# Kernel optimization log

Hardware: AMD Instinct MI355X
Metric: run time of the kernel (lower is better)

## Reference

```python
import jax, jax.numpy as jnp
import numpy as np


def setup_inputs() -> dict:
    key = jax.random.key(0)
    ks = jax.random.split(key, 6)
    B, n_tok, n_RoI = 8, 64, 100
    T_hidden, I_hidden = 768, 1024
    P = I_hidden // 2  # projection = 512
    s_q = 1.0 / np.sqrt(T_hidden)
    s_k = 1.0 / np.sqrt(I_hidden)
    s_w = 1.0 / np.sqrt(P)
    return {
        "encT": jax.random.normal(ks[0], (B, n_tok, T_hidden), jnp.float32),
        "encI": jax.random.normal(ks[1], (B, n_RoI, I_hidden), jnp.float32),
        "mask": jnp.zeros((B, 1, n_tok, n_RoI), jnp.float32),
        "Wq": jax.random.normal(ks[2], (T_hidden, P), jnp.float32) * s_q,
        "bq": jnp.zeros((P,), jnp.float32),
        "Wk": jax.random.normal(ks[3], (I_hidden, P), jnp.float32) * s_k,
        "bk": jnp.zeros((P,), jnp.float32),
        "w": jax.random.normal(ks[4], (P,), jnp.float32) * s_w,
        "b": jnp.zeros((1,), jnp.float32),
    }


def reference(encT, encI, mask, Wq, bq, Wk, bk, w, b):
    # Q_mlp / K_mlp: Linear + exact GELU (torch nn.GELU default)
    q = jax.nn.gelu(jnp.einsum('bth,hp->btp', encT, Wq) + bq, approximate=False)  # [B,T,P]
    k = jax.nn.gelu(jnp.einsum('brh,hp->brp', encI, Wk) + bk, approximate=False)  # [B,R,P]
    # broadcast add (instead of repeat/view), tanh, then Linear(P,1)
    fusion = jnp.tanh(q[:, :, None, :] + k[:, None, :, :])  # [B,T,R,P]
    logits = jnp.einsum('btrp,p->btr', fusion, w) + b[0]      # [B,T,R]
    return logits + jnp.squeeze(mask, axis=1)
```

## Files before the change

kernel.cpp:

```cpp
#include <hip/hip_runtime.h>
#include <hip/hip_fp16.h>
#include <math.h>

#define B_  8
#define T_  64
#define R_  100
#define TH_ 768
#define IH_ 1024
#define P_  512
#define N_  512

#define CTANH 2.88539008177792681f

typedef short short8  __attribute__((ext_vector_type(8)));
typedef float floatx4 __attribute__((ext_vector_type(4)));

__device__ __forceinline__ ushort f2bf(float f) {
  union { float f; unsigned int u; } v; v.f = f;
  unsigned int r = v.u + 0x7FFFu + ((v.u >> 16) & 1u);
  return (ushort)(r >> 16);
}

#define PADK 40

__global__ __launch_bounds__(1024) void mfma_linear_gelu_sk4(
    const float* __restrict__ encT, const float* __restrict__ Wq,
    const float* __restrict__ bq, __half* __restrict__ qout,
    const float* __restrict__ encI, const float* __restrict__ Wk,
    const float* __restrict__ bk, __half* __restrict__ kout) {
  const int rt = blockIdx.y;
  const bool isQ = rt < 8;
  const float* __restrict__ X = isQ ? encT : encI;
  const float* __restrict__ W = isQ ? Wq : Wk;
  const float* __restrict__ bias = isQ ? bq : bk;
  __half* __restrict__ Y = isQ ? qout : kout;
  const int M    = isQ ? (B_ * T_) : (B_ * R_);
  const int KDIM = isQ ? TH_ : IH_;
  const int row0 = (isQ ? rt : (rt - 8)) * 64;
  const int col0 = blockIdx.x * 32;
  const int kq   = KDIM >> 2;
  const int ntiles = kq / 32;

  __shared__ ushort As[4][64 * PADK];
  __shared__ ushort Bs[4][32 * PADK];
  __shared__ float  red[2][64 * 33];

  const int tid = threadIdx.x;
  const int sp  = tid >> 8;
  const int t   = tid & 255;
  const int kbase = sp * kq;

  const int arow = t >> 2;
  const int akq  = (t & 3) * 8;
  const int arowc = min(row0 + arow, M - 1);
  const float* __restrict__ Xp = X + (size_t)arowc * KDIM + kbase + akq;

  const int bkp = (t >> 4) * 2;
  const int bn2 = (t & 15) * 2;
  const float* __restrict__ Wp = W + (size_t)(kbase + bkp) * N_ + col0 + bn2;

  const int wv = t >> 6;
  const int lane = t & 63;
  const int wm = wv * 16;
  const int l15 = lane & 15;
  const int q8  = (lane >> 4) * 8;
  const int q4  = (lane >> 4) * 4;

  floatx4 acc0 = {0.f,0.f,0.f,0.f}, acc1 = {0.f,0.f,0.f,0.f};

  float4 a0 = *(const float4*)(Xp);
  float4 a1 = *(const float4*)(Xp + 4);
  float2 b0 = *(const float2*)(Wp);
  float2 b1 = *(const float2*)(Wp + N_);

  for (int kt = 0; kt < ntiles; ++kt) {
    {
      short8 pk;
      pk[0] = (short)f2bf(a0.x); pk[1] = (short)f2bf(a0.y);
      pk[2] = (short)f2bf(a0.z); pk[3] = (short)f2bf(a0.w);
      pk[4] = (short)f2bf(a1.x); pk[5] = (short)f2bf(a1.y);
      pk[6] = (short)f2bf(a1.z); pk[7] = (short)f2bf(a1.w);
      *(short8*)&As[sp][arow * PADK + akq] = pk;
    }
    {
      unsigned int p0 = (unsigned int)f2bf(b0.x) | ((unsigned int)f2bf(b1.x) << 16);
      unsigned int p1 = (unsigned int)f2bf(b0.y) | ((unsigned int)f2bf(b1.y) << 16);
      *(unsigned int*)&Bs[sp][(bn2 + 0) * PADK + bkp] = p0;
      *(unsigned int*)&Bs[sp][(bn2 + 1) * PADK + bkp] = p1;
    }
    __syncthreads();

    if (kt + 1 < ntiles) {
      const int kb = (kt + 1) * 32;
      a0 = *(const float4*)(Xp + kb);
      a1 = *(const float4*)(Xp + kb + 4);
      b0 = *(const float2*)(Wp + (size_t)kb * N_);
      b1 = *(const float2*)(Wp + (size_t)(kb + 1) * N_);
    }

    short8 af  = *(const short8*)&As[sp][(wm + l15) * PADK + q8];
    short8 bf0 = *(const short8*)&Bs[sp][(l15) * PADK + q8];
    short8 bf1 = *(const short8*)&Bs[sp][(16 + l15) * PADK + q8];
    acc0 = __builtin_amdgcn_mfma_f32_16x16x32_bf16(af, bf0, acc0, 0, 0, 0);
    acc1 = __builtin_amdgcn_mfma_f32_16x16x32_bf16(af, bf1, acc1, 0, 0, 0);
    __syncthreads();
  }

  if (sp >= 2) {
    float* L = red[sp - 2];
    #pragma unroll
    for (int j = 0; j < 4; ++j) {
      L[(wm + q4 + j) * 33 + l15]      = acc0[j];
      L[(wm + q4 + j) * 33 + 16 + l15] = acc1[j];
    }
  }
  __syncthreads();
  if (sp < 2) {
    const float* L = red[sp];
    #pragma unroll
    for (int j = 0; j < 4; ++j) {
      acc0[j] += L[(wm + q4 + j) * 33 + l15];
      acc1[j] += L[(wm + q4 + j) * 33 + 16 + l15];
    }
  }
  __syncthreads();
  if (sp == 1) {
    float* L = red[0];
    #pragma unroll
    for (int j = 0; j < 4; ++j) {
      L[(wm + q4 + j) * 33 + l15]      = acc0[j];
      L[(wm + q4 + j) * 33 + 16 + l15] = acc1[j];
    }
  }
  __syncthreads();
  if (sp == 0) {
    const float* L = red[0];
    const float is2 = 0.70710678118654752f;
    const float bia0 = bias[col0 + l15];
    const float bia1 = bias[col0 + 16 + l15];
    #pragma unroll
    for (int j = 0; j < 4; ++j) {
      const int row = row0 + wm + q4 + j;
      if (row < M) {
        float v0 = acc0[j] + L[(wm + q4 + j) * 33 + l15] + bia0;
        float v1 = acc1[j] + L[(wm + q4 + j) * 33 + 16 + l15] + bia1;
        v0 = CTANH * 0.5f * v0 * (1.f + erff(v0 * is2));
        v1 = CTANH * 0.5f * v1 * (1.f + erff(v1 * is2));
        Y[(size_t)row * N_ + col0 + l15]      = __float2half(v0);
        Y[(size_t)row * N_ + col0 + 16 + l15] = __float2half(v1);
      }
    }
  }
}

__global__ __launch_bounds__(256) void fuse_kernel_h(
    const __half* __restrict__ q, const __half* __restrict__ k,
    const float* __restrict__ w, const float* __restrict__ bscalar,
    const float* __restrict__ mask, float* __restrict__ out) {
  const int bt = blockIdx.x;
  const int wave = threadIdx.x >> 6;
  const int rg = blockIdx.y * 4 + wave;
  if (rg >= 25) return;
  const int lane = threadIdx.x & 63;
  const int sub  = lane >> 4;
  const int pi   = lane & 15;
  const int r = rg * 4 + sub;
  const int b = bt >> 6;

  const __half* __restrict__ qp = q + (size_t)bt * P_ + pi * 8;
  const __half* __restrict__ kp = k + (size_t)(b * R_ + r) * P_ + pi * 8;
  const float* __restrict__ wp = w + pi * 8;

  float acc0 = 0.f, acc1 = 0.f;
  #pragma unroll
  for (int i = 0; i < 4; ++i) {
    union { float4 f; __half2 h[4]; } qu, ku;
    qu.f = *(const float4*)(qp + i * 128);
    ku.f = *(const float4*)(kp + i * 128);
    float4 w0 = *(const float4*)(wp + i * 128);
    float4 w1 = *(const float4*)(wp + i * 128 + 4);
    #pragma unroll
    for (int e = 0; e < 4; ++e) {
      __half2 s = __hadd2(qu.h[e], ku.h[e]);
      float x0 = __low2float(s);
      float x1 = __high2float(s);
      float d0 = __builtin_amdgcn_rcpf(1.f + __builtin_amdgcn_exp2f(x0));
      float d1 = __builtin_amdgcn_rcpf(1.f + __builtin_amdgcn_exp2f(x1));
      float s0 = fmaf(-2.f, d0, 1.f);
      float s1 = fmaf(-2.f, d1, 1.f);
      const float we0 = (e == 0) ? w0.x : (e == 1) ? w0.z : (e == 2) ? w1.x : w1.z;
      const float we1 = (e == 0) ? w0.y : (e == 1) ? w0.w : (e == 2) ? w1.y : w1.w;
      acc0 = fmaf(we0, s0, acc0);
      acc1 = fmaf(we1, s1, acc1);
    }
  }
  float acc = acc0 + acc1;
  #pragma unroll
  for (int off = 1; off < 16; off <<= 1) acc += __shfl_xor(acc, off, 64);

  if (pi == 0) {
    out[(size_t)bt * R_ + r] = acc + bscalar[0] + mask[(size_t)bt * R_ + r];
  }
}

extern "C" void kernel_launch(void* const* d_in, const int* in_sizes, int n_in,
                              void* d_out, int out_size, void* d_ws, size_t ws_size,
                              hipStream_t stream) {
  const float* encT = (const float*)d_in[0];
  const float* encI = (const float*)d_in[1];
  const float* mask = (const float*)d_in[2];
  const float* Wq   = (const float*)d_in[3];
  const float* bq   = (const float*)d_in[4];
  const float* Wk   = (const float*)d_in[5];
  const float* bk   = (const float*)d_in[6];
  const float* w    = (const float*)d_in[7];
  const float* bsc  = (const float*)d_in[8];
  float* out = (float*)d_out;

  __half* q = (__half*)d_ws;
  __half* k = q + (size_t)B_ * T_ * P_;

  dim3 grid(N_ / 32, 8 + 13);
  mfma_linear_gelu_sk4<<<grid, 1024, 0, stream>>>(encT, Wq, bq, q,
                                                  encI, Wk, bk, k);

  fuse_kernel_h<<<dim3(512, 7), 256, 0, stream>>>(q, k, w, bsc, mask, out);
}
```

Before: 95.86 us.

## Tile fusion kernel over 16 tokens with shared-memory q and hoisted weight sum

Each block of the fuse kernel now stages 16 query rows in shared memory and gives each wave one RoI. The wave holds its k row and w slice in registers and reuses them across the 16 tokens. The tanh-weighted sum is rewritten algebraically as sum(w) - 2*sum(w*d), which drops the per-element fma for 1-2d and precomputes sum(w) once. Each token now needs a full 64-lane shuffle reduction, 16 times per wave, which adds cross-lane work compared with the old 16-lane reduction.

```diff
diff --git a/kernel.cpp b/kernel.cpp
--- a/kernel.cpp
+++ b/kernel.cpp
@@ -153,32 +153,46 @@
   }
 }
 
-__global__ __launch_bounds__(256) void fuse_kernel_h(
+__global__ __launch_bounds__(256) void fuse_kernel_t16(
     const __half* __restrict__ q, const __half* __restrict__ k,
     const float* __restrict__ w, const float* __restrict__ bscalar,
     const float* __restrict__ mask, float* __restrict__ out) {
-  const int bt = blockIdx.x;
+  const int bx = blockIdx.x;
+  const int b  = bx >> 2;
+  const int t0 = (bx & 3) * 16;
   const int wave = threadIdx.x >> 6;
-  const int rg = blockIdx.y * 4 + wave;
-  if (rg >= 25) return;
   const int lane = threadIdx.x & 63;
-  const int sub  = lane >> 4;
-  const int pi   = lane & 15;
-  const int r = rg * 4 + sub;
-  const int b = bt >> 6;
-
-  const __half* __restrict__ qp = q + (size_t)bt * P_ + pi * 8;
-  const __half* __restrict__ kp = k + (size_t)(b * R_ + r) * P_ + pi * 8;
-  const float* __restrict__ wp = w + pi * 8;
-
-  float acc0 = 0.f, acc1 = 0.f;
+  const int r = blockIdx.y * 4 + wave;
+
+  __shared__ __half qs[16 * 512];
+
+  {
+    const float4* __restrict__ src =
+        (const float4*)(q + (size_t)(b * 64 + t0) * 512);
+    float4* dst = (float4*)qs;
+    #pragma unroll
+    for (int i = 0; i < 4; ++i)
+      dst[threadIdx.x + 256 * i] = src[threadIdx.x + 256 * i];
+  }
+
+  union { float4 f; __half2 h[4]; } ku;
+  ku.f = *(const float4*)(k + ((size_t)(b * R_ + r) << 9) + lane * 8);
+
+  float wr[8];
+  *(float4*)&wr[0] = *(const float4*)(w + lane * 8);
+  *(float4*)&wr[4] = *(const float4*)(w + lane * 8 + 4);
+  float sumw = wr[0] + wr[1] + wr[2] + wr[3] + wr[4] + wr[5] + wr[6] + wr[7];
   #pragma unroll
-  for (int i = 0; i < 4; ++i) {
-    union { float4 f; __half2 h[4]; } qu, ku;
-    qu.f = *(const float4*)(qp + i * 128);
-    ku.f = *(const float4*)(kp + i * 128);
-    float4 w0 = *(const float4*)(wp + i * 128);
-    float4 w1 = *(const float4*)(wp + i * 128 + 4);
+  for (int off = 1; off < 64; off <<= 1) sumw += __shfl_xor(sumw, off, 64);
+
+  __syncthreads();
+
+  float res = 0.f;
+  #pragma unroll
+  for (int tt = 0; tt < 16; ++tt) {
+    union { float4 f; __half2 h[4]; } qu;
+    qu.f = *(const float4*)(qs + tt * 512 + lane * 8);
+    float accd0 = 0.f, accd1 = 0.f;
     #pragma unroll
     for (int e = 0; e < 4; ++e) {
       __half2 s = __hadd2(qu.h[e], ku.h[e]);
@@ -186,20 +200,19 @@
       float x1 = __high2float(s);
       float d0 = __builtin_amdgcn_rcpf(1.f + __builtin_amdgcn_exp2f(x0));
       float d1 = __builtin_amdgcn_rcpf(1.f + __builtin_amdgcn_exp2f(x1));
-      float s0 = fmaf(-2.f, d0, 1.f);
-      float s1 = fmaf(-2.f, d1, 1.f);
-      const float we0 = (e == 0) ? w0.x : (e == 1) ? w0.z : (e == 2) ? w1.x : w1.z;
-      const float we1 = (e == 0) ? w0.y : (e == 1) ? w0.w : (e == 2) ? w1.y : w1.w;
-      acc0 = fmaf(we0, s0, acc0);
-      acc1 = fmaf(we1, s1, acc1);
-    }
-  }
-  float acc = acc0 + acc1;
-  #pragma unroll
-  for (int off = 1; off < 16; off <<= 1) acc += __shfl_xor(acc, off, 64);
-
-  if (pi == 0) {
-    out[(size_t)bt * R_ + r] = acc + bscalar[0] + mask[(size_t)bt * R_ + r];
+      accd0 = fmaf(wr[2 * e],     d0, accd0);
+      accd1 = fmaf(wr[2 * e + 1], d1, accd1);
+    }
+    float accd = accd0 + accd1;
+    #pragma unroll
+    for (int off = 1; off < 64; off <<= 1) accd += __shfl_xor(accd, off, 64);
+    res = (lane == tt) ? accd : res;
+  }
+
+  if (lane < 16) {
+    const int bt = b * 64 + t0 + lane;
+    const size_t o = (size_t)bt * R_ + r;
+    out[o] = sumw - 2.f * res + bscalar[0] + mask[o];
   }
 }
 
@@ -224,5 +237,5 @@
   mfma_linear_gelu_sk4<<<grid, 1024, 0, stream>>>(encT, Wq, bq, q,
                                                   encI, Wk, bk, k);
 
-  fuse_kernel_h<<<dim3(512, 7), 256, 0, stream>>>(q, k, w, bsc, mask, out);
-}
+  fuse_kernel_t16<<<dim3(32, 25), 256, 0, stream>>>(q, k, w, bsc, mask, out);
+}
```

After: 98.46 us. 2.7% more time.
